# Kernel optimization log

Hardware: AMD Instinct MI355X
Metric: run time of the kernel (lower is better)

Reference implementation:

```python
import jax, jax.numpy as jnp
import numpy as np

K = 23          # tagset size
START = 1
END = 2
NEG = -10000.0


def _lstm_dir(x, Wih, Whh, b, reverse):
    # x: [B,T,E]; Wih: [4H,E]; Whh: [4H,H]; b: [4H] (b_ih + b_hh fused)
    B = x.shape[0]
    H = Whh.shape[1]
    h0 = jnp.zeros((B, H), x.dtype)
    c0 = jnp.zeros((B, H), x.dtype)

    def step(hc, xt):
        h, c = hc
        g = xt @ Wih.T + h @ Whh.T + b          # [B,4H], gate order i,f,g,o (torch)
        i, f, gg, o = jnp.split(g, 4, axis=-1)
        c = jax.nn.sigmoid(f) * c + jax.nn.sigmoid(i) * jnp.tanh(gg)
        h = jax.nn.sigmoid(o) * jnp.tanh(c)
        return (h, c), h

    xs = jnp.swapaxes(x, 0, 1)                   # [T,B,E]
    _, hs = jax.lax.scan(step, (h0, c0), xs, reverse=reverse)
    return jnp.swapaxes(hs, 0, 1)                # [B,T,H]


def _viterbi(feats, seq_len, transitions):
    # feats: [B,T,K]; batched Viterbi with length masking (identity backpointers
    # on padded steps so the DP state freezes at t == seq_len).
    B, T, _ = feats.shape
    init = jnp.full((B, K), NEG, feats.dtype).at[:, START].set(0.0)
    mask = jnp.arange(T)[None, :] < seq_len[:, None]     # [B,T]
    feats_t = jnp.swapaxes(feats, 0, 1)                  # [T,B,K]
    mask_t = mask.T                                      # [T,B]
    ident = jnp.arange(K)[None, :]

    def vit_step(fv, inp):
        ft, mt = inp                                     # [B,K], [B]
        sc = fv[:, None, :] + transitions[None, :, :]    # [B, next, prev]
        bp = jnp.argmax(sc, axis=-1)                     # [B,K]
        best = jnp.max(sc, axis=-1) + ft                 # [B,K]
        fv_new = jnp.where(mt[:, None], best, fv)
        bp = jnp.where(mt[:, None], bp, ident)
        return fv_new, bp

    fv, bps = jax.lax.scan(vit_step, init, (feats_t, mask_t))   # bps: [T,B,K]
    term = fv + transitions[END][None, :]                # [B,K]
    best_tag = jnp.argmax(term, axis=-1)                 # [B]
    score = jnp.max(term, axis=-1)                       # [B]

    def back_step(tag, bp_t):
        new = jnp.take_along_axis(bp_t, tag[:, None], axis=1)[:, 0]
        return new, new

    # path[T-1] = best_tag; path[t] = bps[t+1][path[t+1]]
    _, prevs = jax.lax.scan(back_step, best_tag, bps[1:], reverse=True)  # [T-1,B]
    paths = jnp.concatenate([prevs, best_tag[None, :]], axis=0).T        # [B,T]
    return score, paths


def setup_inputs() -> dict:
    key = jax.random.key(0)
    ks = jax.random.split(key, 12)
    B, T, E, HD = 64, 512, 512, 1024
    H = HD // 2
    s = 1.0 / np.sqrt(H)
    u = lambda k, shp: jax.random.uniform(k, shp, jnp.float32, -s, s)
    texts = jax.random.normal(ks[0], (B, T, E), jnp.float32)
    seq_len = jax.random.randint(ks[1], (B,), 1, T + 1)
    transitions = jax.random.normal(ks[10], (K, K), jnp.float32)
    transitions = transitions.at[START, :].set(NEG).at[:, END].set(NEG)
    return {
        'texts': texts, 'seq_len': seq_len,
        'Wih_f': u(ks[2], (4 * H, E)), 'Whh_f': u(ks[3], (4 * H, H)), 'b_f': u(ks[4], (4 * H,)),
        'Wih_b': u(ks[5], (4 * H, E)), 'Whh_b': u(ks[6], (4 * H, H)), 'b_b': u(ks[7], (4 * H,)),
        'W_h2t': u(ks[8], (K, HD)), 'b_h2t': u(ks[9], (K,)),
        'transitions': transitions,
    }


def reference(texts, seq_len, Wih_f, Whh_f, b_f, Wih_b, Whh_b, b_b, W_h2t, b_h2t, transitions):
    h_fwd = _lstm_dir(texts, Wih_f, Whh_f, b_f, reverse=False)
    h_bwd = _lstm_dir(texts, Wih_b, Whh_b, b_b, reverse=True)
    lstm_out = jnp.concatenate([h_fwd, h_bwd], axis=-1)      # [B,T,hidden_dim]
    feats = lstm_out @ W_h2t.T + b_h2t                        # [B,T,K] emissions
    scores, paths = _viterbi(feats, seq_len, transitions)
    return scores, paths
```

## Files before the change

### kernel.cpp

```cpp
#include <hip/hip_runtime.h>
#include <stdint.h>
#include <math.h>

#define T_LEN 512
#define BATCH 64
#define EMB   512
#define HID   512
#define NTAG  23
#define NEGV  -10000.0f

typedef __attribute__((ext_vector_type(4))) float f32x4;
typedef __attribute__((ext_vector_type(8))) short short8;

#define DEVI __device__ __forceinline__

DEVI unsigned short f32_to_bf16_rn(float f) {
  union { float f; uint32_t u; } v; v.f = f;
  uint32_t u = v.u;
  uint32_t r = u + 0x7FFFu + ((u >> 16) & 1u);
  return (unsigned short)(r >> 16);
}
DEVI float bf16_to_f32(unsigned short h) {
  union { float f; uint32_t u; } v; v.u = ((uint32_t)h) << 16;
  return v.f;
}

DEVI f32x4 mfma16(short8 a, short8 b, f32x4 c) {
  return __builtin_amdgcn_mfma_f32_16x16x32_bf16(a, b, c, 0, 0, 0);
}

DEVI void ld_sc(const void* p, short8& d) {
  asm volatile("global_load_dwordx4 %0, %1, off sc1" : "=v"(d) : "v"(p) : "memory");
}
DEVI void wait_all(short8& a0, short8& a1, short8& a2, short8& a3,
                   short8& b0, short8& b1, short8& b2, short8& b3) {
  asm volatile("s_waitcnt vmcnt(0)"
               : "+v"(a0), "+v"(a1), "+v"(a2), "+v"(a3),
                 "+v"(b0), "+v"(b1), "+v"(b2), "+v"(b3)
               :: "memory");
}

DEVI float fast_sigmoid(float x) {
  float e = exp2f(x * -1.44269504f);
  return __builtin_amdgcn_rcpf(1.0f + e);
}
DEVI float fast_tanh(float x) {
  float xc = fminf(fmaxf(x, -20.0f), 20.0f);
  float t = exp2f(xc * -2.88539008f);
  return (1.0f - t) * __builtin_amdgcn_rcpf(1.0f + t);
}

__global__ __launch_bounds__(256) void prep_xf(const float* __restrict__ x,
                                               unsigned short* __restrict__ xf_hi,
                                               unsigned short* __restrict__ xf_lo) {
  int idx = blockIdx.x * 256 + threadIdx.x;
  int lane = idx & 63;
  int kq   = (idx >> 6) & 15;
  int mt   = (idx >> 10) & 3;
  int t    = idx >> 12;
  int b  = mt * 16 + (lane & 15);
  int e0 = kq * 32 + (lane >> 4) * 8;
  const float* src = x + ((size_t)b * T_LEN + t) * EMB + e0;
  size_t dst = (size_t)idx * 8;
#pragma unroll
  for (int i = 0; i < 8; ++i) {
    float v = src[i];
    unsigned short hi = f32_to_bf16_rn(v);
    unsigned short lo = f32_to_bf16_rn(v - bf16_to_f32(hi));
    xf_hi[dst + i] = hi;
    xf_lo[dst + i] = lo;
  }
}

__global__ __launch_bounds__(256) void prep_wf(const float* __restrict__ whh_f,
                                               const float* __restrict__ wih_f,
                                               const float* __restrict__ whh_b,
                                               const float* __restrict__ wih_b,
                                               unsigned short* __restrict__ wf_hi,
                                               unsigned short* __restrict__ wf_lo) {
  int idx = blockIdx.x * 256 + threadIdx.x;
  int lane = idx & 63;
  int kq   = (idx >> 6) & 15;
  int nt   = (idx >> 10) & 3;
  int js   = (idx >> 12) & 31;
  int mat  = (idx >> 17) & 1;
  int dir  = (idx >> 18) & 1;
  const float* W = dir ? (mat ? wih_b : whh_b) : (mat ? wih_f : whh_f);
  int row = nt * 512 + js * 16 + (lane & 15);
  int k0  = kq * 32 + (lane >> 4) * 8;
  const float* src = W + (size_t)row * 512 + k0;
  size_t dst = (size_t)idx * 8;
#pragma unroll
  for (int i = 0; i < 8; ++i) {
    float v = src[i];
    unsigned short hi = f32_to_bf16_rn(v);
    unsigned short lo = f32_to_bf16_rn(v - bf16_to_f32(hi));
    wf_hi[dst + i] = hi;
    wf_lo[dst + i] = lo;
  }
}

__global__ __launch_bounds__(256) void prep_w2t(const float* __restrict__ w2t,
                                                unsigned short* __restrict__ o_hi,
                                                unsigned short* __restrict__ o_lo) {
  int idx = blockIdx.x * 256 + threadIdx.x;
  int lane = idx & 63;
  int kq   = (idx >> 6) & 31;
  int nt   = (idx >> 11) & 1;
  int n  = nt * 16 + (lane & 15);
  int k0 = kq * 32 + (lane >> 4) * 8;
  size_t dst = (size_t)idx * 8;
#pragma unroll
  for (int i = 0; i < 8; ++i) {
    float v = (n < NTAG) ? w2t[(size_t)n * 1024 + k0 + i] : 0.0f;
    unsigned short hi = f32_to_bf16_rn(v);
    unsigned short lo = f32_to_bf16_rn(v - bf16_to_f32(hi));
    o_hi[dst + i] = hi;
    o_lo[dst + i] = lo;
  }
}

__global__ __launch_bounds__(256) void fill_sent(uint4* __restrict__ hi,
                                                 uint4* __restrict__ lo) {
  const uint4 v = {0x7F807F80u, 0x7F807F80u, 0x7F807F80u, 0x7F807F80u};
  unsigned idx = blockIdx.x * 256 + threadIdx.x;
#pragma unroll
  for (int i = 0; i < 4; ++i) {
    unsigned k = idx + (unsigned)i * 1048576u;
    unsigned word = k << 2;
    unsigned dir  = word >> 23;
    unsigned rem  = word & 8388607u;
    unsigned slot = 1u + (rem >> 14);
    unsigned off  = rem & 16383u;
    size_t dst = (((size_t)(dir * 514 + slot) << 14) + off) >> 2;
    hi[dst] = v;
    lo[dst] = v;
  }
}

__global__ __launch_bounds__(256, 1)
void lstm_rec(const unsigned short* __restrict__ xf_hi,
              const unsigned short* __restrict__ xf_lo,
              const unsigned short* __restrict__ wf_hi,
              const unsigned short* __restrict__ wf_lo,
              const float* __restrict__ bias_f,
              const float* __restrict__ bias_b,
              unsigned short* __restrict__ hf_hi,
              unsigned short* __restrict__ hf_lo) {
  extern __shared__ unsigned char smem[];
  unsigned short* w_lds = (unsigned short*)smem;
  float* scratch = (float*)(smem + 131072);

  int wg  = blockIdx.x;
  int dir = wg >> 7;
  int js  = (wg >> 2) & 31;
  int bq  = wg & 3;
  int tid  = threadIdx.x;
  int wave = tid >> 6;
  int lane = tid & 63;

  {
    const uint4* s0 = (const uint4*)wf_hi + ((size_t)(dir * 2 + 0) * 32 + js) * 4096;
    const uint4* s1 = (const uint4*)wf_hi + ((size_t)(dir * 2 + 1) * 32 + js) * 4096;
    uint4* d = (uint4*)w_lds;
    for (int i = tid; i < 4096; i += 256) { d[i] = s0[i]; d[4096 + i] = s1[i]; }
  }

  short8 wlo_h[4][4], wlo_x[4][4];
#pragma unroll
  for (int q = 0; q < 4; ++q) {
    int kq = wave * 4 + q;
#pragma unroll
    for (int nt = 0; nt < 4; ++nt) {
      wlo_h[q][nt] = *(const short8*)(wf_lo +
            ((((((size_t)dir * 2 + 0) * 32 + js) * 4 + nt) * 16 + kq) * 64 + lane) * 8);
      wlo_x[q][nt] = *(const short8*)(wf_lo +
            ((((((size_t)dir * 2 + 1) * 32 + js) * 4 + nt) * 16 + kq) * 64 + lane) * 8);
    }
  }
  __syncthreads();

  int sm = tid >> 4;
  int sj = tid & 15;
  int jglob = js * 16 + sj;
  const float* bias = dir ? bias_b : bias_f;
  float bias_g[4];
#pragma unroll
  for (int g = 0; g < 4; ++g) bias_g[g] = bias[g * 512 + jglob];
  float c_state = 0.0f;

  int kqh   = jglob >> 5;
  int lane2 = ((jglob >> 3) & 3) * 16 + sm;
  int jrem  = jglob & 7;

  for (int s = 0; s < T_LEN; ++s) {
    int t = dir ? (T_LEN - 1 - s) : s;
    int rslot = dir ? (t + 2) : t;

    f32x4 acc[4];
#pragma unroll
    for (int nt = 0; nt < 4; ++nt) { f32x4 z = {0.f, 0.f, 0.f, 0.f}; acc[nt] = z; }

    short8 xh[4], xl[4];
#pragma unroll
    for (int q = 0; q < 4; ++q) {
      int kq = wave * 4 + q;
      size_t xoff = ((((size_t)t * 4 + bq) * 16 + kq) * 64 + lane) * 8;
      xh[q] = *(const short8*)(xf_hi + xoff);
      xl[q] = *(const short8*)(xf_lo + xoff);
    }
#pragma unroll
    for (int q = 0; q < 4; ++q) {
      int kq = wave * 4 + q;
#pragma unroll
      for (int nt = 0; nt < 4; ++nt) {
        short8 bh = *(const short8*)&w_lds[((((size_t)(1 * 4 + nt)) * 16 + kq) * 64 + lane) * 8];
        acc[nt] = mfma16(xh[q], bh, acc[nt]);
        acc[nt] = mfma16(xh[q], wlo_x[q][nt], acc[nt]);
        acc[nt] = mfma16(xl[q], bh, acc[nt]);
      }
    }

    short8 hh[4], hl[4];
    {
      const short8* bhp = (const short8*)hf_hi + ((((size_t)dir * 514 + rslot) * 4 + bq) * 16) * 64;
      const short8* blp = (const short8*)hf_lo + ((((size_t)dir * 514 + rslot) * 4 + bq) * 16) * 64;
      int guard = 0;
      for (;;) {
#pragma unroll
        for (int q = 0; q < 4; ++q) {
          int kq = wave * 4 + q;
          ld_sc((const void*)(bhp + kq * 64 + lane), hh[q]);
          ld_sc((const void*)(blp + kq * 64 + lane), hl[q]);
        }
        wait_all(hh[0], hh[1], hh[2], hh[3], hl[0], hl[1], hl[2], hl[3]);
        uint32_t bad = 0;
#pragma unroll
        for (int q = 0; q < 4; ++q) {
          const uint32_t* wh = (const uint32_t*)&hh[q];
          const uint32_t* wl = (const uint32_t*)&hl[q];
#pragma unroll
          for (int i = 0; i < 4; ++i) {
            uint32_t x = wh[i] ^ 0x7F807F80u;
            bad |= (x - 0x00010001u) & ~x & 0x80008000u;
            uint32_t y = wl[i] ^ 0x7F807F80u;
            bad |= (y - 0x00010001u) & ~y & 0x80008000u;
          }
        }
        if (__ballot(bad != 0) == 0ull) break;
        if (++guard > 2000000) break;
        __builtin_amdgcn_s_sleep(1);
      }
    }

#pragma unroll
    for (int q = 0; q < 4; ++q) {
      int kq = wave * 4 + q;
#pragma unroll
      for (int nt = 0; nt < 4; ++nt) {
        short8 bh = *(const short8*)&w_lds[((((size_t)(0 * 4 + nt)) * 16 + kq) * 64 + lane) * 8];
        acc[nt] = mfma16(hh[q], bh, acc[nt]);
        acc[nt] = mfma16(hh[q], wlo_h[q][nt], acc[nt]);
        acc[nt] = mfma16(hl[q], bh, acc[nt]);
      }
    }

#pragma unroll
    for (int nt = 0; nt < 4; ++nt)
      *(f32x4*)&scratch[((size_t)(wave * 4 + nt) * 64 + lane) * 4] = acc[nt];
    __syncthreads();

    int lidx = (((sm >> 2) * 16) + sj) * 4 + (sm & 3);
    float g4[4];
#pragma unroll
    for (int g = 0; g < 4; ++g) {
      float v = bias_g[g];
#pragma unroll
      for (int w = 0; w < 4; ++w) v += scratch[(w * 4 + g) * 256 + lidx];
      g4[g] = v;
    }
    __syncthreads();

    float i_s = fast_sigmoid(g4[0]);
    float f_s = fast_sigmoid(g4[1]);
    float g_t = fast_tanh(g4[2]);
    float o_s = fast_sigmoid(g4[3]);
    c_state = f_s * c_state + i_s * g_t;
    float h = o_s * fast_tanh(c_state);

    unsigned int vhi = f32_to_bf16_rn(h);
    unsigned int vlo = f32_to_bf16_rn(h - bf16_to_f32((unsigned short)vhi));
    unsigned int phi = (unsigned int)__shfl_xor((int)vhi, 1);
    unsigned int plo = (unsigned int)__shfl_xor((int)vlo, 1);
    if ((sj & 1) == 0) {
      unsigned int whi = vhi | (phi << 16);
      unsigned int wlo = vlo | (plo << 16);
      size_t foff = ((((size_t)dir * 514 + (t + 1)) * 4 + bq) * 16 + kqh);
      size_t eoff = (foff * 64 + lane2) * 8 + jrem;
      __hip_atomic_store((unsigned int*)(hf_hi + eoff), whi,
                         __ATOMIC_RELAXED, __HIP_MEMORY_SCOPE_AGENT);
      __hip_atomic_store((unsigned int*)(hf_lo + eoff), wlo,
                         __ATOMIC_RELAXED, __HIP_MEMORY_SCOPE_AGENT);
    }
  }
}

__global__ __launch_bounds__(256) void feats_kernel(const unsigned short* __restrict__ hf_hi,
                                                    const unsigned short* __restrict__ hf_lo,
                                                    const unsigned short* __restrict__ w2t_hi,
                                                    const unsigned short* __restrict__ w2t_lo,
                                                    const float* __restrict__ b_h2t,
                                                    float* __restrict__ feats) {
  int t = blockIdx.x;
  int wave = threadIdx.x >> 6;
  int lane = threadIdx.x & 63;
  f32x4 acc[2];
#pragma unroll
  for (int nt = 0; nt < 2; ++nt) { f32x4 z = {0.f, 0.f, 0.f, 0.f}; acc[nt] = z; }

  for (int kq = 0; kq < 32; ++kq) {
    int dir = kq >> 4, kqi = kq & 15;
    size_t af = (((((size_t)dir * 514 + (t + 1)) * 4 + wave) * 16 + kqi) * 64 + lane) * 8;
    short8 ah = *(const short8*)(hf_hi + af);
    short8 al = *(const short8*)(hf_lo + af);
#pragma unroll
    for (int nt = 0; nt < 2; ++nt) {
      size_t bf = (((size_t)nt * 32 + kq) * 64 + lane) * 8;
      short8 bh = *(const short8*)(w2t_hi + bf);
      short8 bl = *(const short8*)(w2t_lo + bf);
      acc[nt] = mfma16(ah, bh, acc[nt]);
      acc[nt] = mfma16(ah, bl, acc[nt]);
      acc[nt] = mfma16(al, bh, acc[nt]);
    }
  }
  int quad = lane >> 4, col = lane & 15;
#pragma unroll
  for (int nt = 0; nt < 2; ++nt) {
    int n = nt * 16 + col;
    if (n < NTAG) {
      float bb = b_h2t[n];
#pragma unroll
      for (int r = 0; r < 4; ++r) {
        int b = wave * 16 + quad * 4 + r;
        feats[((size_t)b * T_LEN + t) * 24 + n] = acc[nt][r] + bb;
      }
    }
  }
}

__global__ __launch_bounds__(64) void viterbi_kernel(const float* __restrict__ feats,
                                                     const int* __restrict__ seq_len,
                                                     const float* __restrict__ trans,
                                                     float* __restrict__ out) {
  int b = blockIdx.x;
  int lane = threadIdx.x;
  __shared__ unsigned char bp_s[T_LEN * 24];
  bool tag_lane = lane < NTAG;
  float tr_reg[NTAG];
#pragma unroll 1
  for (int k = 0; k < NTAG; ++k) tr_reg[k] = tag_lane ? trans[lane * NTAG + k] : NEGV;
  float fv = (lane == 1) ? 0.0f : NEGV;
  int L = seq_len[b];
  float ft = tag_lane ? feats[((size_t)b * T_LEN) * 24 + lane] : 0.0f;
#pragma unroll 1
  for (int t = 0; t < T_LEN; ++t) {
    float ftn = 0.0f;
    if (t + 1 < T_LEN && tag_lane) ftn = feats[((size_t)b * T_LEN + t + 1) * 24 + lane];
    float best = __shfl(fv, 0) + tr_reg[0];
    int arg = 0;
#pragma unroll 1
    for (int k = 1; k < NTAG; ++k) {
      float v = __shfl(fv, k) + tr_reg[k];
      if (v > best) { best = v; arg = k; }
    }
    bool active = (t < L);
    if (tag_lane) bp_s[t * 24 + lane] = (unsigned char)(active ? arg : lane);
    fv = active ? (best + ft) : fv;
    ft = ftn;
  }
  float term = tag_lane ? (fv + trans[2 * NTAG + lane]) : NEGV;
  float bv = term; int bi = lane;
#pragma unroll
  for (int off = 32; off; off >>= 1) {
    float ov = __shfl_down(bv, off);
    int oi = __shfl_down(bi, off);
    if (ov > bv || (ov == bv && oi < bi)) { bv = ov; bi = oi; }
  }
  __syncthreads();
  if (lane == 0) {
    out[b] = bv;
    int tag = bi;
    out[64 + (size_t)b * T_LEN + (T_LEN - 1)] = (float)tag;
    for (int t = T_LEN - 2; t >= 0; --t) {
      tag = bp_s[(t + 1) * 24 + tag];
      out[64 + (size_t)b * T_LEN + t] = (float)tag;
    }
  }
}

extern "C" void kernel_launch(void* const* d_in, const int* in_sizes, int n_in,
                              void* d_out, int out_size, void* d_ws, size_t ws_size,
                              hipStream_t stream) {
  const float* texts   = (const float*)d_in[0];
  const int*   seq_len = (const int*)d_in[1];
  const float* Wih_f   = (const float*)d_in[2];
  const float* Whh_f   = (const float*)d_in[3];
  const float* b_f     = (const float*)d_in[4];
  const float* Wih_b   = (const float*)d_in[5];
  const float* Whh_b   = (const float*)d_in[6];
  const float* b_b     = (const float*)d_in[7];
  const float* W_h2t   = (const float*)d_in[8];
  const float* b_h2t   = (const float*)d_in[9];
  const float* trans   = (const float*)d_in[10];
  (void)in_sizes; (void)n_in; (void)out_size; (void)ws_size;

  unsigned char* ws = (unsigned char*)d_ws;
  size_t off = 0;
  auto alloc = [&](size_t bytes) -> void* {
    void* p = ws + off;
    off += (bytes + 255) & ~(size_t)255;
    return p;
  };
  unsigned short* xf_hi  = (unsigned short*)alloc(33554432);
  unsigned short* xf_lo  = (unsigned short*)alloc(33554432);
  unsigned short* wf_hi  = (unsigned short*)alloc(8388608);
  unsigned short* wf_lo  = (unsigned short*)alloc(8388608);
  unsigned short* hf_hi  = (unsigned short*)alloc(67371008);
  unsigned short* hf_lo  = (unsigned short*)alloc(67371008);
  unsigned short* w2t_hi = (unsigned short*)alloc(65536);
  unsigned short* w2t_lo = (unsigned short*)alloc(65536);
  float*          feats  = (float*)alloc(3145728);

  for (int d = 0; d < 2; ++d) {
    hipMemsetAsync(hf_hi + ((size_t)d * 514 + 0)   * 32768, 0, 65536, stream);
    hipMemsetAsync(hf_hi + ((size_t)d * 514 + 513) * 32768, 0, 65536, stream);
    hipMemsetAsync(hf_lo + ((size_t)d * 514 + 0)   * 32768, 0, 65536, stream);
    hipMemsetAsync(hf_lo + ((size_t)d * 514 + 513) * 32768, 0, 65536, stream);
  }

  hipFuncSetAttribute((const void*)lstm_rec,
                      hipFuncAttributeMaxDynamicSharedMemorySize, 147456);

  fill_sent<<<4096, 256, 0, stream>>>((uint4*)hf_hi, (uint4*)hf_lo);
  prep_xf<<<8192, 256, 0, stream>>>(texts, xf_hi, xf_lo);
  prep_wf<<<2048, 256, 0, stream>>>(Whh_f, Wih_f, Whh_b, Wih_b, wf_hi, wf_lo);
  prep_w2t<<<16, 256, 0, stream>>>(W_h2t, w2t_hi, w2t_lo);
  lstm_rec<<<256, 256, 147456, stream>>>(xf_hi, xf_lo, wf_hi, wf_lo,
                                         b_f, b_b, hf_hi, hf_lo);
  feats_kernel<<<512, 256, 0, stream>>>(hf_hi, hf_lo, w2t_hi, w2t_lo, b_h2t, feats);
  viterbi_kernel<<<64, 64, 0, stream>>>(feats, seq_len, trans, (float*)d_out);
}
```

Before: 2.648 ms.

## Issue recurrent h loads before input-projection MFMAs and coalesce prep_xf reads

The step loop now issues the polled hidden-state loads together with the x-fragment loads, then waits only for the x loads (vmcnt 8). This lets the h-load latency overlap the input-projection MFMAs, and the spin loop reloads only when data is still unready. The prep_xf kernel also reads contiguous float4 pairs per lane and remaps the output lane index, so global reads coalesce. This relies on the hardware returning loads in issue order for the vmcnt(8) wait to be correct, and the early h loads may see stale data more often, which costs extra poll iterations.

```diff
diff --git a/kernel.cpp b/kernel.cpp
--- a/kernel.cpp
+++ b/kernel.cpp
@@ -32,9 +32,19 @@
 DEVI void ld_sc(const void* p, short8& d) {
   asm volatile("global_load_dwordx4 %0, %1, off sc1" : "=v"(d) : "v"(p) : "memory");
 }
+DEVI void ld_l2(const void* p, short8& d) {
+  asm volatile("global_load_dwordx4 %0, %1, off" : "=v"(d) : "v"(p) : "memory");
+}
 DEVI void wait_all(short8& a0, short8& a1, short8& a2, short8& a3,
                    short8& b0, short8& b1, short8& b2, short8& b3) {
   asm volatile("s_waitcnt vmcnt(0)"
+               : "+v"(a0), "+v"(a1), "+v"(a2), "+v"(a3),
+                 "+v"(b0), "+v"(b1), "+v"(b2), "+v"(b3)
+               :: "memory");
+}
+DEVI void wait_vmcnt8(short8& a0, short8& a1, short8& a2, short8& a3,
+                      short8& b0, short8& b1, short8& b2, short8& b3) {
+  asm volatile("s_waitcnt vmcnt(8)"
                : "+v"(a0), "+v"(a1), "+v"(a2), "+v"(a3),
                  "+v"(b0), "+v"(b1), "+v"(b2), "+v"(b3)
                :: "memory");
@@ -58,13 +68,18 @@
   int kq   = (idx >> 6) & 15;
   int mt   = (idx >> 10) & 3;
   int t    = idx >> 12;
-  int b  = mt * 16 + (lane & 15);
-  int e0 = kq * 32 + (lane >> 4) * 8;
-  const float* src = x + ((size_t)b * T_LEN + t) * EMB + e0;
-  size_t dst = (size_t)idx * 8;
+  int bl = lane >> 2;
+  int eo = lane & 3;
+  int b  = mt * 16 + bl;
+  int e0 = kq * 32 + eo * 8;
+  const float4* src = (const float4*)(x + ((size_t)b * T_LEN + t) * EMB + e0);
+  float4 v0 = src[0], v1 = src[1];
+  float vv[8] = {v0.x, v0.y, v0.z, v0.w, v1.x, v1.y, v1.z, v1.w};
+  int lf = eo * 16 + bl;
+  size_t dst = ((size_t)(idx >> 6) * 64 + lf) * 8;
 #pragma unroll
   for (int i = 0; i < 8; ++i) {
-    float v = src[i];
+    float v = vv[i];
     unsigned short hi = f32_to_bf16_rn(v);
     unsigned short lo = f32_to_bf16_rn(v - bf16_to_f32(hi));
     xf_hi[dst + i] = hi;
@@ -201,14 +216,25 @@
 #pragma unroll
     for (int nt = 0; nt < 4; ++nt) { f32x4 z = {0.f, 0.f, 0.f, 0.f}; acc[nt] = z; }
 
-    short8 xh[4], xl[4];
+    const short8* bhp = (const short8*)hf_hi + ((((size_t)dir * 514 + rslot) * 4 + bq) * 16) * 64;
+    const short8* blp = (const short8*)hf_lo + ((((size_t)dir * 514 + rslot) * 4 + bq) * 16) * 64;
+
+    short8 xh[4], xl[4], hh[4], hl[4];
 #pragma unroll
     for (int q = 0; q < 4; ++q) {
       int kq = wave * 4 + q;
       size_t xoff = ((((size_t)t * 4 + bq) * 16 + kq) * 64 + lane) * 8;
-      xh[q] = *(const short8*)(xf_hi + xoff);
-      xl[q] = *(const short8*)(xf_lo + xoff);
-    }
+      ld_l2((const void*)(xf_hi + xoff), xh[q]);
+      ld_l2((const void*)(xf_lo + xoff), xl[q]);
+    }
+#pragma unroll
+    for (int q = 0; q < 4; ++q) {
+      int kq = wave * 4 + q;
+      ld_sc((const void*)(bhp + kq * 64 + lane), hh[q]);
+      ld_sc((const void*)(blp + kq * 64 + lane), hl[q]);
+    }
+    wait_vmcnt8(xh[0], xh[1], xh[2], xh[3], xl[0], xl[1], xl[2], xl[3]);
+
 #pragma unroll
     for (int q = 0; q < 4; ++q) {
       int kq = wave * 4 + q;
@@ -221,19 +247,10 @@
       }
     }
 
-    short8 hh[4], hl[4];
     {
-      const short8* bhp = (const short8*)hf_hi + ((((size_t)dir * 514 + rslot) * 4 + bq) * 16) * 64;
-      const short8* blp = (const short8*)hf_lo + ((((size_t)dir * 514 + rslot) * 4 + bq) * 16) * 64;
+      wait_all(hh[0], hh[1], hh[2], hh[3], hl[0], hl[1], hl[2], hl[3]);
       int guard = 0;
       for (;;) {
-#pragma unroll
-        for (int q = 0; q < 4; ++q) {
-          int kq = wave * 4 + q;
-          ld_sc((const void*)(bhp + kq * 64 + lane), hh[q]);
-          ld_sc((const void*)(blp + kq * 64 + lane), hl[q]);
-        }
-        wait_all(hh[0], hh[1], hh[2], hh[3], hl[0], hl[1], hl[2], hl[3]);
         uint32_t bad = 0;
 #pragma unroll
         for (int q = 0; q < 4; ++q) {
@@ -250,6 +267,13 @@
         if (__ballot(bad != 0) == 0ull) break;
         if (++guard > 2000000) break;
         __builtin_amdgcn_s_sleep(1);
+#pragma unroll
+        for (int q = 0; q < 4; ++q) {
+          int kq = wave * 4 + q;
+          ld_sc((const void*)(bhp + kq * 64 + lane), hh[q]);
+          ld_sc((const void*)(blp + kq * 64 + lane), hl[q]);
+        }
+        wait_all(hh[0], hh[1], hh[2], hh[3], hl[0], hl[1], hl[2], hl[3]);
       }
     }
 
```

Result: faster. 2.138 ms (-19.3%).
